# Optimization experiments

Hardware: AMD Instinct MI355X
Metric: run time of the kernel (lower is better)

The kernel has to match this reference:

```python
import jax, jax.numpy as jnp
import numpy as np

B, T, E, H, C = 32, 128, 256, 256, 16

def setup_inputs() -> dict:
    key = jax.random.key(0)
    ks = jax.random.split(key, 16)
    def p(k, shape, scale=0.05):
        return jax.random.normal(k, shape, dtype=jnp.float32) * scale
    return {
        "x": jax.random.normal(ks[0], (B, T, E), dtype=jnp.float32),
        "W_in": p(ks[1], (H, E)), "b_in": p(ks[2], (H,)),
        "Wih": p(ks[3], (3 * H, H)), "bih": p(ks[4], (3 * H,)),
        "Whh": p(ks[5], (3 * H, H)), "bhh": p(ks[6], (3 * H,)),
        "Wa": p(ks[7], (H, H)), "ba": p(ks[8], (H,)),
        "Ua": p(ks[9], (H, H)), "ub": p(ks[10], (H,)),
        "va_w": p(ks[11], (1, H)), "va_b": p(ks[12], (1,)),
        "Wo": p(ks[13], (C, 2 * H)), "bo": p(ks[14], (C,)),
    }

def reference(x, W_in, b_in, Wih, bih, Whh, bhh, Wa, ba, Ua, ub, va_w, va_b, Wo, bo):
    # linear_in (+ Identity activation): x -> [B,T,H]
    xp = x @ W_in.T + b_in
    xp_t = jnp.transpose(xp, (1, 0, 2))          # [T,B,H], time-major
    # Precompute per-step GRU input projections and attention key projections
    xw = xp_t @ Wih.T + bih                      # [T,B,3H]
    uax = xp_t @ Ua.T + ub                       # [T,B,H]
    ts = jnp.arange(T)

    def gru_step(h, xw_t):
        # PyTorch GRU cell: gate order r, z, n
        hw = h @ Whh.T + bhh                     # [B,3H]
        xr, xz, xn = jnp.split(xw_t, 3, axis=-1)
        hr, hz, hn = jnp.split(hw, 3, axis=-1)
        r = jax.nn.sigmoid(xr + hr)
        z = jax.nn.sigmoid(xz + hz)
        n = jnp.tanh(xn + r * hn)
        return (1.0 - z) * n + z * h

    def outer_step(h_prev, i):
        # Re-run RNN over prefix x[:, :i+1] starting from the CARRIED hidden,
        # exactly as the torch loop does (hidden is not reset between iters).
        def inner(h, inp):
            t, xw_t = inp
            hn = gru_step(h, xw_t)
            h = jnp.where(t <= i, hn, h)         # freeze past the prefix end
            return h, h
        h_last, outs = jax.lax.scan(inner, h_prev, (ts, xw))  # outs [T,B,H]
        # Bahdanau attention: query = rnn outputs, keys = linear_in outputs
        s = jnp.tanh(outs @ Wa.T + ba + uax)     # [T,B,H]
        scores = jnp.squeeze(s @ va_w.T, -1) + va_b  # [T,B]
        scores = jnp.where((ts <= i)[:, None], scores, -1e9)
        w = jax.nn.softmax(scores, axis=0)       # softmax over prefix positions
        context = jnp.einsum('tb,tbh->bh', w, xp_t)
        cats = jnp.concatenate([h_last, context], axis=-1)  # [B,2H]
        return h_last, cats @ Wo.T + bo          # logits [B,C]

    h0 = jnp.zeros((x.shape[0], H), dtype=x.dtype)
    _, logits = jax.lax.scan(outer_step, h0, ts)  # [T,B,C]
    return jax.nn.sigmoid(jnp.transpose(logits, (1, 0, 2)))  # [B,T,C]
```

## Files before the change

kernel.cpp:

```cpp
#include <hip/hip_runtime.h>

constexpr int NB = 32;
constexpr int NT = 128;
constexpr int NE = 256;
constexpr int NH = 256;
constexpr int NC = 16;

typedef _Float16 f16;
typedef f16 f16x2 __attribute__((ext_vector_type(2)));
typedef f16 f16x8 __attribute__((ext_vector_type(8)));

__device__ __forceinline__ float sigmoidf_(float x) {
    return 1.f / (1.f + __expf(-x));
}
__device__ __forceinline__ float tanhf_(float x) {
    x = fminf(fmaxf(x, -15.f), 15.f);
    float e = __expf(-2.f * x);
    return (1.f - e) / (1.f + e);
}
__device__ __forceinline__ float dot4_(float4 a, float4 b) {
    return a.x * b.x + a.y * b.y + a.z * b.z + a.w * b.w;
}
#if __has_builtin(__builtin_amdgcn_fdot2)
__device__ __forceinline__ float fdot2_(f16x2 a, f16x2 b, float c) {
    return __builtin_amdgcn_fdot2(a, b, c, false);
}
#else
__device__ __forceinline__ float fdot2_(f16x2 a, f16x2 b, float c) {
    return (float)a[0] * (float)b[0] + (float)a[1] * (float)b[1] + c;
}
#endif
#define PAIR(v, k) __builtin_shufflevector((v), (v), (k), (k) + 1)

__global__ __launch_bounds__(256) void k_lin_in(
    const float* __restrict__ x, const float* __restrict__ W_in,
    const float* __restrict__ b_in, float* __restrict__ xp) {
    const int tb = blockIdx.x;
    const int t = tb >> 5, b = tb & 31;
    const int tid = threadIdx.x;
    __shared__ __align__(16) float xl[NE];
    xl[tid] = x[(b * NT + t) * NE + tid];
    __syncthreads();
    const float* __restrict__ wr = W_in + tid * NE;
    float acc = b_in[tid];
#pragma unroll 8
    for (int k = 0; k < NE; k += 4)
        acc += dot4_(*(const float4*)(wr + k), *(const float4*)(xl + k));
    xp[tb * NH + tid] = acc;
}

__global__ __launch_bounds__(256) void k_proj(
    const float* __restrict__ xp, const float* __restrict__ Wih,
    const float* __restrict__ bih, const float* __restrict__ Ua,
    const float* __restrict__ ub, float* __restrict__ xw,
    float* __restrict__ uax) {
    const int tb = blockIdx.x;
    const int tid = threadIdx.x;
    __shared__ __align__(16) float xl[NH];
    xl[tid] = xp[tb * NH + tid];
    __syncthreads();
    const float* __restrict__ wr = Wih + tid * NH;
    const float* __restrict__ wz = Wih + (NH + tid) * NH;
    const float* __restrict__ wn = Wih + (2 * NH + tid) * NH;
    const float* __restrict__ wu = Ua + tid * NH;
    float ar = bih[tid], az = bih[NH + tid], an = bih[2 * NH + tid], au = ub[tid];
#pragma unroll 4
    for (int k = 0; k < NH; k += 4) {
        float4 xv = *(const float4*)(xl + k);
        ar += dot4_(*(const float4*)(wr + k), xv);
        az += dot4_(*(const float4*)(wz + k), xv);
        an += dot4_(*(const float4*)(wn + k), xv);
        au += dot4_(*(const float4*)(wu + k), xv);
    }
    float* xwp = xw + tb * (3 * NH);
    xwp[tid] = ar;
    xwp[NH + tid] = az;
    xwp[2 * NH + tid] = an;
    uax[tb * NH + tid] = au;
}

__global__ __launch_bounds__(256) void k_pack(
    const float* __restrict__ Whh, const float* __restrict__ Wa,
    f16x8* __restrict__ Wpk, f16x8* __restrict__ Wak) {
    const int id = blockIdx.x * 256 + threadIdx.x;
    if (id < 32 * 768) {
        const int kc = id / 768, row = id % 768;
        const float* src = Whh + row * NH + kc * 8;
        f16x8 v;
#pragma unroll
        for (int m = 0; m < 8; ++m) v[m] = (f16)src[m];
        Wpk[id] = v;
    } else {
        const int id2 = id - 32 * 768;
        const int kc = id2 >> 8, row = id2 & 255;
        const float* src = Wa + row * NH + kc * 8;
        f16x8 v;
#pragma unroll
        for (int m = 0; m < 8; ++m) v[m] = (f16)src[m];
        Wak[id2] = v;
    }
}

__global__ __attribute__((amdgpu_waves_per_eu(4, 4))) __launch_bounds__(1024)
void k_chain(
    const float* __restrict__ Whh, const float* __restrict__ bhh,
    const float* __restrict__ xw, float* __restrict__ Hc) {
    const int b = blockIdx.x;
    const int tid = threadIdx.x;
    const int j = tid >> 2, c = tid & 3;
    __shared__ __align__(16) f16 hb[2][4 * 72];

    f16x2 wr[32], wz[32], wn[32];
    {
        const float2* pr = (const float2*)(Whh + (size_t)(0 * NH + j) * NH + c * 64);
        const float2* pz = (const float2*)(Whh + (size_t)(1 * NH + j) * NH + c * 64);
        const float2* pn = (const float2*)(Whh + (size_t)(2 * NH + j) * NH + c * 64);
#pragma unroll
        for (int m = 0; m < 32; ++m) {
            float2 a = pr[m]; wr[m] = f16x2{(f16)a.x, (f16)a.y};
            float2 d = pz[m]; wz[m] = f16x2{(f16)d.x, (f16)d.y};
            float2 e = pn[m]; wn[m] = f16x2{(f16)e.x, (f16)e.y};
        }
    }
    const float bhr = bhh[j], bhz = bhh[NH + j], bhn = bhh[2 * NH + j];
    if (tid < NH) hb[0][(tid >> 6) * 72 + (tid & 63)] = (f16)0.f;
    float hprev = 0.f;
    int cur = 0;
    __syncthreads();

#pragma unroll 1
    for (int i = 0; i < NT; ++i) {
#pragma unroll 1
        for (int t = 0; t <= i; ++t) {
            const float* __restrict__ xwp = xw + (size_t)(t * NB + b) * (3 * NH);
            const float xr = xwp[j], xz = xwp[NH + j], xn = xwp[2 * NH + j];
            const f16* hc = hb[cur] + c * 72;
            float ar = 0.f, az = 0.f, an = 0.f;
#pragma unroll
            for (int s = 0; s < 8; ++s) {
                const f16x8 hv = *(const f16x8*)(hc + s * 8);
                const f16x2 h0 = PAIR(hv, 0), h1 = PAIR(hv, 2),
                            h2 = PAIR(hv, 4), h3 = PAIR(hv, 6);
                ar = fdot2_(wr[s * 4 + 0], h0, ar);
                ar = fdot2_(wr[s * 4 + 1], h1, ar);
                ar = fdot2_(wr[s * 4 + 2], h2, ar);
                ar = fdot2_(wr[s * 4 + 3], h3, ar);
                az = fdot2_(wz[s * 4 + 0], h0, az);
                az = fdot2_(wz[s * 4 + 1], h1, az);
                az = fdot2_(wz[s * 4 + 2], h2, az);
                az = fdot2_(wz[s * 4 + 3], h3, az);
                an = fdot2_(wn[s * 4 + 0], h0, an);
                an = fdot2_(wn[s * 4 + 1], h1, an);
                an = fdot2_(wn[s * 4 + 2], h2, an);
                an = fdot2_(wn[s * 4 + 3], h3, an);
            }
            ar += __shfl_xor(ar, 1); ar += __shfl_xor(ar, 2);
            az += __shfl_xor(az, 1); az += __shfl_xor(az, 2);
            an += __shfl_xor(an, 1); an += __shfl_xor(an, 2);
            const float r = sigmoidf_(xr + ar + bhr);
            const float z = sigmoidf_(xz + az + bhz);
            const float n = tanhf_(xn + r * (an + bhn));
            const float hnew = (1.f - z) * n + z * hprev;
            hprev = hnew;
            if (c == 0) {
                hb[cur ^ 1][(j >> 6) * 72 + (j & 63)] = (f16)hnew;
                if (t == i) Hc[((size_t)i * NB + b) * NH + j] = hnew;
            }
            cur ^= 1;
            __syncthreads();
        }
    }
}

__global__ __attribute__((amdgpu_waves_per_eu(2, 2))) __launch_bounds__(512)
void k_attn(
    const float* __restrict__ Hc, const float* __restrict__ xw,
    const float* __restrict__ uax, const float* __restrict__ xp,
    const f16x8* __restrict__ Wpk, const f16x8* __restrict__ Wak,
    const float* __restrict__ bhh, const float* __restrict__ ba,
    const float* __restrict__ va_w, const float* __restrict__ Wo,
    const float* __restrict__ bo, float* __restrict__ out) {
    const int b  = blockIdx.x >> 3;
    const int bk = blockIdx.x & 7;
    const int tid = threadIdx.x;
    const int col = tid >> 1, c = tid & 1;
    const int lane = tid & 63, wid = tid >> 6;

    __shared__ __align__(16) float S[16][NH];
    __shared__ __align__(16) f16 Sh[16][NH];
    __shared__ float red1[8][16];
    __shared__ float mL[16], lL[16], aL[16], eL[16];
    __shared__ float redH[8][256];

    const float bhr = bhh[col], bhz = bhh[NH + col], bhn = bhh[2 * NH + col];
    const float ba_j = ba[col], va_j = va_w[col];
    float ctx[16];
#pragma unroll
    for (int u = 0; u < 16; ++u) {
        const int ic = bk + 8 * u;
        const float hv = (ic == 0) ? 0.f : Hc[((size_t)(ic - 1) * NB + b) * NH + col];
        if (c == 0) { S[u][col] = hv; Sh[u][col] = (f16)hv; }
        ctx[u] = 0.f;
    }
    if (tid < 16) { mL[tid] = -1e30f; lL[tid] = 0.f; }
    __syncthreads();

    const int imax = bk + 8 * 15;
#pragma unroll 1
    for (int t = 0; t <= imax; ++t) {
        const size_t base = (size_t)(t * NB + b);
        const float xr = xw[base * 3 * NH + col];
        const float xz = xw[base * 3 * NH + NH + col];
        const float xn = xw[base * 3 * NH + 2 * NH + col];
        const float ux = uax[base * NH + col];
        const float xpt = xp[base * NH + col];

        float ar[16], az[16], an[16];
#pragma unroll
        for (int u = 0; u < 16; ++u) { ar[u] = 0.f; az[u] = 0.f; an[u] = 0.f; }
#pragma unroll 2
        for (int kk = 0; kk < 16; ++kk) {
            const int kc = kk * 2 + c;
            const f16x8 wR = Wpk[kc * 768 + col];
            const f16x8 wZ = Wpk[kc * 768 + 256 + col];
            const f16x8 wN = Wpk[kc * 768 + 512 + col];
#pragma unroll
            for (int u = 0; u < 16; ++u) {
                if (bk + 8 * u < t) continue;
                const f16x8 hv = *(const f16x8*)&Sh[u][kc * 8];
                const f16x2 h0 = PAIR(hv, 0), h1 = PAIR(hv, 2),
                            h2 = PAIR(hv, 4), h3 = PAIR(hv, 6);
                ar[u] = fdot2_(PAIR(wR, 0), h0, ar[u]);
                ar[u] = fdot2_(PAIR(wR, 2), h1, ar[u]);
                ar[u] = fdot2_(PAIR(wR, 4), h2, ar[u]);
                ar[u] = fdot2_(PAIR(wR, 6), h3, ar[u]);
                az[u] = fdot2_(PAIR(wZ, 0), h0, az[u]);
                az[u] = fdot2_(PAIR(wZ, 2), h1, az[u]);
                az[u] = fdot2_(PAIR(wZ, 4), h2, az[u]);
                az[u] = fdot2_(PAIR(wZ, 6), h3, az[u]);
                an[u] = fdot2_(PAIR(wN, 0), h0, an[u]);
                an[u] = fdot2_(PAIR(wN, 2), h1, an[u]);
                an[u] = fdot2_(PAIR(wN, 4), h2, an[u]);
                an[u] = fdot2_(PAIR(wN, 6), h3, an[u]);
            }
        }
        float hn[16];
#pragma unroll
        for (int u = 0; u < 16; ++u) {
            if (bk + 8 * u < t) continue;
            float arf = ar[u] + __shfl_xor(ar[u], 1);
            float azf = az[u] + __shfl_xor(az[u], 1);
            float anf = an[u] + __shfl_xor(an[u], 1);
            const float r = sigmoidf_(xr + arf + bhr);
            const float z = sigmoidf_(xz + azf + bhz);
            const float n = tanhf_(xn + r * (anf + bhn));
            hn[u] = (1.f - z) * n + z * S[u][col];
        }
        __syncthreads();
#pragma unroll
        for (int u = 0; u < 16; ++u) {
            if (bk + 8 * u < t) continue;
            if (c == 0) { S[u][col] = hn[u]; Sh[u][col] = (f16)hn[u]; }
        }
        __syncthreads();

        float sc[16];
#pragma unroll
        for (int u = 0; u < 16; ++u) sc[u] = 0.f;
#pragma unroll 2
        for (int kk = 0; kk < 16; ++kk) {
            const int kc = kk * 2 + c;
            const f16x8 wA = Wak[kc * 256 + col];
#pragma unroll
            for (int u = 0; u < 16; ++u) {
                if (bk + 8 * u < t) continue;
                const f16x8 hv = *(const f16x8*)&Sh[u][kc * 8];
                sc[u] = fdot2_(PAIR(wA, 0), PAIR(hv, 0), sc[u]);
                sc[u] = fdot2_(PAIR(wA, 2), PAIR(hv, 2), sc[u]);
                sc[u] = fdot2_(PAIR(wA, 4), PAIR(hv, 4), sc[u]);
                sc[u] = fdot2_(PAIR(wA, 6), PAIR(hv, 6), sc[u]);
            }
        }
#pragma unroll
        for (int u = 0; u < 16; ++u) {
            if (bk + 8 * u < t) continue;
            const float sv = sc[u] + __shfl_xor(sc[u], 1);
            float p = (c == 0) ? va_j * tanhf_(sv + ba_j + ux) : 0.f;
#pragma unroll
            for (int off = 32; off; off >>= 1) p += __shfl_xor(p, off);
            if (lane == 0) red1[wid][u] = p;
        }
        __syncthreads();
        if (tid < 16 && bk + 8 * tid >= t) {
            float s = 0.f;
#pragma unroll
            for (int w = 0; w < 8; ++w) s += red1[w][tid];
            const float mo = mL[tid];
            const float mn = fmaxf(mo, s);
            const float e  = __expf(s - mn);
            const float al = __expf(mo - mn);
            lL[tid] = lL[tid] * al + e;
            mL[tid] = mn; aL[tid] = al; eL[tid] = e;
        }
        __syncthreads();
#pragma unroll
        for (int u = 0; u < 16; ++u) {
            if (bk + 8 * u < t) continue;
            ctx[u] = ctx[u] * aL[u] + eL[u] * xpt;
        }
    }

#pragma unroll 1
    for (int u = 0; u < 16; ++u) {
        const float hl = S[u][col];
        const float cx = ctx[u] / lL[u];
#pragma unroll
        for (int cls = 0; cls < NC; ++cls) {
            float p = Wo[cls * (2 * NH) + col] * hl + Wo[cls * (2 * NH) + NH + col] * cx;
            p = (c == 0) ? p : 0.f;
#pragma unroll
            for (int off = 32; off; off >>= 1) p += __shfl_xor(p, off);
            if (lane == 0) redH[wid][u * 16 + cls] = p;
        }
    }
    __syncthreads();
    if (tid < 256) {
        const int u = tid >> 4, cls = tid & 15;
        const int ic = bk + 8 * u;
        float lg = bo[cls];
#pragma unroll
        for (int w = 0; w < 8; ++w) lg += redH[w][tid];
        out[((size_t)b * NT + ic) * NC + cls] = sigmoidf_(lg);
    }
}

extern "C" void kernel_launch(void* const* d_in, const int* in_sizes, int n_in,
                              void* d_out, int out_size, void* d_ws, size_t ws_size,
                              hipStream_t stream) {
    (void)in_sizes; (void)n_in; (void)out_size; (void)ws_size;
    const float* x    = (const float*)d_in[0];
    const float* W_in = (const float*)d_in[1];
    const float* b_in = (const float*)d_in[2];
    const float* Wih  = (const float*)d_in[3];
    const float* bih  = (const float*)d_in[4];
    const float* Whh  = (const float*)d_in[5];
    const float* bhh  = (const float*)d_in[6];
    const float* Wa   = (const float*)d_in[7];
    const float* ba   = (const float*)d_in[8];
    const float* Ua   = (const float*)d_in[9];
    const float* ub   = (const float*)d_in[10];
    const float* va_w = (const float*)d_in[11];
    const float* Wo   = (const float*)d_in[13];
    const float* bo   = (const float*)d_in[14];
    float* out = (float*)d_out;

    float* ws  = (float*)d_ws;
    float* xp  = ws;
    float* xw  = xp  + (size_t)NT * NB * NH;
    float* uax = xw  + (size_t)NT * NB * 3 * NH;
    float* Hc  = uax + (size_t)NT * NB * NH;
    f16x8* Wpk = (f16x8*)(Hc + (size_t)NT * NB * NH);
    f16x8* Wak = Wpk + 32 * 768;

    hipLaunchKernelGGL(k_lin_in, dim3(NT * NB), dim3(256), 0, stream, x, W_in, b_in, xp);
    hipLaunchKernelGGL(k_proj,   dim3(NT * NB), dim3(256), 0, stream, xp, Wih, bih, Ua, ub, xw, uax);
    hipLaunchKernelGGL(k_pack,   dim3(128),     dim3(256), 0, stream, Whh, Wa, Wpk, Wak);
    hipLaunchKernelGGL(k_chain,  dim3(NB),      dim3(1024), 0, stream, Whh, bhh, xw, Hc);
    hipLaunchKernelGGL(k_attn,   dim3(NB * 8),  dim3(512), 0, stream,
                       Hc, xw, uax, xp, Wpk, Wak, bhh, ba, va_w, Wo, bo, out);
}
```

Baseline: 16.09 ms.

## Move GRU n-gate weights to LDS and software-prefetch weights in attention kernel

In the serial chain kernel, the n-gate recurrent weights move from per-thread registers into a padded shared-memory buffer, and the waves_per_eu occupancy attribute is removed, which lowers register pressure. In the attention kernel, the weight loads for the next k-chunk are issued one iteration ahead (register double-buffering) with unroll 1, and its occupancy attribute is removed as well. The intent is to avoid register spills in the latency-bound chain and to hide global load latency in the attention kernel. In exchange, the chain adds LDS reads and about 140KB of shared memory per block, and the prefetch adds live registers.

```diff
diff --git a/kernel.cpp b/kernel.cpp
--- a/kernel.cpp
+++ b/kernel.cpp
@@ -101,25 +101,29 @@
     }
 }
 
-__global__ __attribute__((amdgpu_waves_per_eu(4, 4))) __launch_bounds__(1024)
-void k_chain(
+__global__ __launch_bounds__(1024) void k_chain(
     const float* __restrict__ Whh, const float* __restrict__ bhh,
     const float* __restrict__ xw, float* __restrict__ Hc) {
     const int b = blockIdx.x;
     const int tid = threadIdx.x;
     const int j = tid >> 2, c = tid & 3;
+
+    __shared__ __align__(16) f16x2 WnL[256 * 140];
     __shared__ __align__(16) f16 hb[2][4 * 72];
 
-    f16x2 wr[32], wz[32], wn[32];
+    for (int e = tid; e < 256 * 128; e += 1024) {
+        const int row = e >> 7, q = e & 127;
+        const float2 v = *(const float2*)(Whh + (size_t)(2 * NH + row) * NH + q * 2);
+        WnL[row * 140 + q] = f16x2{(f16)v.x, (f16)v.y};
+    }
+    f16x2 wr[32], wz[32];
     {
         const float2* pr = (const float2*)(Whh + (size_t)(0 * NH + j) * NH + c * 64);
         const float2* pz = (const float2*)(Whh + (size_t)(1 * NH + j) * NH + c * 64);
-        const float2* pn = (const float2*)(Whh + (size_t)(2 * NH + j) * NH + c * 64);
 #pragma unroll
         for (int m = 0; m < 32; ++m) {
             float2 a = pr[m]; wr[m] = f16x2{(f16)a.x, (f16)a.y};
             float2 d = pz[m]; wz[m] = f16x2{(f16)d.x, (f16)d.y};
-            float2 e = pn[m]; wn[m] = f16x2{(f16)e.x, (f16)e.y};
         }
     }
     const float bhr = bhh[j], bhz = bhh[NH + j], bhn = bhh[2 * NH + j];
@@ -127,6 +131,8 @@
     float hprev = 0.f;
     int cur = 0;
     __syncthreads();
+
+    const f16x2* __restrict__ wnp = WnL + j * 140 + c * 32;
 
 #pragma unroll 1
     for (int i = 0; i < NT; ++i) {
@@ -139,6 +145,7 @@
 #pragma unroll
             for (int s = 0; s < 8; ++s) {
                 const f16x8 hv = *(const f16x8*)(hc + s * 8);
+                const f16x8 wv = *(const f16x8*)(wnp + s * 4);
                 const f16x2 h0 = PAIR(hv, 0), h1 = PAIR(hv, 2),
                             h2 = PAIR(hv, 4), h3 = PAIR(hv, 6);
                 ar = fdot2_(wr[s * 4 + 0], h0, ar);
@@ -149,10 +156,10 @@
                 az = fdot2_(wz[s * 4 + 1], h1, az);
                 az = fdot2_(wz[s * 4 + 2], h2, az);
                 az = fdot2_(wz[s * 4 + 3], h3, az);
-                an = fdot2_(wn[s * 4 + 0], h0, an);
-                an = fdot2_(wn[s * 4 + 1], h1, an);
-                an = fdot2_(wn[s * 4 + 2], h2, an);
-                an = fdot2_(wn[s * 4 + 3], h3, an);
+                an = fdot2_(PAIR(wv, 0), h0, an);
+                an = fdot2_(PAIR(wv, 2), h1, an);
+                an = fdot2_(PAIR(wv, 4), h2, an);
+                an = fdot2_(PAIR(wv, 6), h3, an);
             }
             ar += __shfl_xor(ar, 1); ar += __shfl_xor(ar, 2);
             az += __shfl_xor(az, 1); az += __shfl_xor(az, 2);
@@ -172,8 +179,7 @@
     }
 }
 
-__global__ __attribute__((amdgpu_waves_per_eu(2, 2))) __launch_bounds__(512)
-void k_attn(
+__global__ __launch_bounds__(512) void k_attn(
     const float* __restrict__ Hc, const float* __restrict__ xw,
     const float* __restrict__ uax, const float* __restrict__ xp,
     const f16x8* __restrict__ Wpk, const f16x8* __restrict__ Wak,
@@ -218,30 +224,40 @@
         float ar[16], az[16], an[16];
 #pragma unroll
         for (int u = 0; u < 16; ++u) { ar[u] = 0.f; az[u] = 0.f; an[u] = 0.f; }
-#pragma unroll 2
-        for (int kk = 0; kk < 16; ++kk) {
-            const int kc = kk * 2 + c;
-            const f16x8 wR = Wpk[kc * 768 + col];
-            const f16x8 wZ = Wpk[kc * 768 + 256 + col];
-            const f16x8 wN = Wpk[kc * 768 + 512 + col];
-#pragma unroll
-            for (int u = 0; u < 16; ++u) {
-                if (bk + 8 * u < t) continue;
-                const f16x8 hv = *(const f16x8*)&Sh[u][kc * 8];
-                const f16x2 h0 = PAIR(hv, 0), h1 = PAIR(hv, 2),
-                            h2 = PAIR(hv, 4), h3 = PAIR(hv, 6);
-                ar[u] = fdot2_(PAIR(wR, 0), h0, ar[u]);
-                ar[u] = fdot2_(PAIR(wR, 2), h1, ar[u]);
-                ar[u] = fdot2_(PAIR(wR, 4), h2, ar[u]);
-                ar[u] = fdot2_(PAIR(wR, 6), h3, ar[u]);
-                az[u] = fdot2_(PAIR(wZ, 0), h0, az[u]);
-                az[u] = fdot2_(PAIR(wZ, 2), h1, az[u]);
-                az[u] = fdot2_(PAIR(wZ, 4), h2, az[u]);
-                az[u] = fdot2_(PAIR(wZ, 6), h3, az[u]);
-                an[u] = fdot2_(PAIR(wN, 0), h0, an[u]);
-                an[u] = fdot2_(PAIR(wN, 2), h1, an[u]);
-                an[u] = fdot2_(PAIR(wN, 4), h2, an[u]);
-                an[u] = fdot2_(PAIR(wN, 6), h3, an[u]);
+        {
+            int kc = c;
+            f16x8 wR = Wpk[kc * 768 + col];
+            f16x8 wZ = Wpk[kc * 768 + 256 + col];
+            f16x8 wN = Wpk[kc * 768 + 512 + col];
+#pragma unroll 1
+            for (int kk = 0; kk < 16; ++kk) {
+                const int kcn = kc + 2;
+                f16x8 nR, nZ, nN;
+                if (kk < 15) {
+                    nR = Wpk[kcn * 768 + col];
+                    nZ = Wpk[kcn * 768 + 256 + col];
+                    nN = Wpk[kcn * 768 + 512 + col];
+                }
+#pragma unroll
+                for (int u = 0; u < 16; ++u) {
+                    if (bk + 8 * u < t) continue;
+                    const f16x8 hv = *(const f16x8*)&Sh[u][kc * 8];
+                    const f16x2 h0 = PAIR(hv, 0), h1 = PAIR(hv, 2),
+                                h2 = PAIR(hv, 4), h3 = PAIR(hv, 6);
+                    ar[u] = fdot2_(PAIR(wR, 0), h0, ar[u]);
+                    ar[u] = fdot2_(PAIR(wR, 2), h1, ar[u]);
+                    ar[u] = fdot2_(PAIR(wR, 4), h2, ar[u]);
+                    ar[u] = fdot2_(PAIR(wR, 6), h3, ar[u]);
+                    az[u] = fdot2_(PAIR(wZ, 0), h0, az[u]);
+                    az[u] = fdot2_(PAIR(wZ, 2), h1, az[u]);
+                    az[u] = fdot2_(PAIR(wZ, 4), h2, az[u]);
+                    az[u] = fdot2_(PAIR(wZ, 6), h3, az[u]);
+                    an[u] = fdot2_(PAIR(wN, 0), h0, an[u]);
+                    an[u] = fdot2_(PAIR(wN, 2), h1, an[u]);
+                    an[u] = fdot2_(PAIR(wN, 4), h2, an[u]);
+                    an[u] = fdot2_(PAIR(wN, 6), h3, an[u]);
+                }
+                wR = nR; wZ = nZ; wN = nN; kc = kcn;
             }
         }
         float hn[16];
@@ -267,18 +283,24 @@
         float sc[16];
 #pragma unroll
         for (int u = 0; u < 16; ++u) sc[u] = 0.f;
-#pragma unroll 2
-        for (int kk = 0; kk < 16; ++kk) {
-            const int kc = kk * 2 + c;
-            const f16x8 wA = Wak[kc * 256 + col];
-#pragma unroll
-            for (int u = 0; u < 16; ++u) {
-                if (bk + 8 * u < t) continue;
-                const f16x8 hv = *(const f16x8*)&Sh[u][kc * 8];
-                sc[u] = fdot2_(PAIR(wA, 0), PAIR(hv, 0), sc[u]);
-                sc[u] = fdot2_(PAIR(wA, 2), PAIR(hv, 2), sc[u]);
-                sc[u] = fdot2_(PAIR(wA, 4), PAIR(hv, 4), sc[u]);
-                sc[u] = fdot2_(PAIR(wA, 6), PAIR(hv, 6), sc[u]);
+        {
+            int kc = c;
+            f16x8 wA = Wak[kc * 256 + col];
+#pragma unroll 1
+            for (int kk = 0; kk < 16; ++kk) {
+                const int kcn = kc + 2;
+                f16x8 nA;
+                if (kk < 15) nA = Wak[kcn * 256 + col];
+#pragma unroll
+                for (int u = 0; u < 16; ++u) {
+                    if (bk + 8 * u < t) continue;
+                    const f16x8 hv = *(const f16x8*)&Sh[u][kc * 8];
+                    sc[u] = fdot2_(PAIR(wA, 0), PAIR(hv, 0), sc[u]);
+                    sc[u] = fdot2_(PAIR(wA, 2), PAIR(hv, 2), sc[u]);
+                    sc[u] = fdot2_(PAIR(wA, 4), PAIR(hv, 4), sc[u]);
+                    sc[u] = fdot2_(PAIR(wA, 6), PAIR(hv, 6), sc[u]);
+                }
+                wA = nA; kc = kcn;
             }
         }
 #pragma unroll
```

Result: slower. 16.85 ms (+4.7%).
